# Kernel optimization log

Hardware: AMD Instinct MI355X
Metric: run time of the kernel (lower is better)

## Reference

```python
import jax, jax.numpy as jnp
import numpy as np

EMB = 300
HID = 1024
RELU = 512
NCLS = 3
T = 8192


def _lstm_layer(x, Wih, Whh, bih, bhh):
    # x: [T, in_dim]; PyTorch gate order i, f, g, o; batch = 1 so state is a vector.
    H = Whh.shape[1]
    xg = x @ Wih.T + bih  # [T, 4H], input projection hoisted out of the scan

    def step(carry, xg_t):
        h, c = carry
        gates = xg_t + Whh @ h + bhh
        i, f, g, o = jnp.split(gates, 4)
        i = jax.nn.sigmoid(i)
        f = jax.nn.sigmoid(f)
        g = jnp.tanh(g)
        o = jax.nn.sigmoid(o)
        c = f * c + i * g
        h = o * jnp.tanh(c)
        return (h, c), h

    h0 = jnp.zeros((H,), x.dtype)
    (_, _), hs = jax.lax.scan(step, (h0, h0), xg)
    return hs  # [T, H]


def setup_inputs() -> dict:
    key = jax.random.key(0)
    ks = jax.random.split(key, 16)
    s_lstm = 1.0 / np.sqrt(HID)

    def n(k, shape, s):
        return (jax.random.normal(k, shape, dtype=jnp.float32) * s)

    return {
        "quote": n(ks[0], (T, EMB), 1.0),
        "Wih0": n(ks[1], (4 * HID, EMB), s_lstm),
        "Whh0": n(ks[2], (4 * HID, HID), s_lstm),
        "bih0": n(ks[3], (4 * HID,), s_lstm),
        "bhh0": n(ks[4], (4 * HID,), s_lstm),
        "Wih1": n(ks[5], (4 * HID, HID), s_lstm),
        "Whh1": n(ks[6], (4 * HID, HID), s_lstm),
        "bih1": n(ks[7], (4 * HID,), s_lstm),
        "bhh1": n(ks[8], (4 * HID,), s_lstm),
        "W0": n(ks[9], (RELU, HID), 1.0 / np.sqrt(HID)),
        "b0": n(ks[10], (RELU,), 0.01),
        "W1": n(ks[11], (RELU, RELU), 1.0 / np.sqrt(RELU)),
        "b1": n(ks[12], (RELU,), 0.01),
        "W2": n(ks[13], (NCLS, RELU), 1.0 / np.sqrt(RELU)),
        "b2": n(ks[14], (NCLS,), 0.01),
    }


def reference(quote, Wih0, Whh0, bih0, bhh0, Wih1, Whh1, bih1, bhh1,
              W0, b0, W1, b1, W2, b2):
    h1 = _lstm_layer(quote, Wih0, Whh0, bih0, bhh0)  # [T, HID]
    h2 = _lstm_layer(h1, Wih1, Whh1, bih1, bhh1)     # [T, HID]
    last = h2[-1]                                     # lstmOut of final word, batch 1
    x = jax.nn.relu(last @ W0.T + b0)
    x = jax.nn.relu(x @ W1.T + b1)
    # Dropout(p=0.5) is identity in eval mode.
    logits = (x @ W2.T + b2).reshape(1, NCLS)
    return jax.nn.log_softmax(logits, axis=1)
```

## Files before the change

kernel.cpp:

```cpp
#include <hip/hip_runtime.h>
#include <stdint.h>

typedef unsigned int uint32;
typedef unsigned long long uint64;

#define T_SEQ 8192

#define WO_WHH0  0ull
#define WO_WIH0  8388608ull
#define WO_WHH1  10878976ull
#define WO_WIH1  19267584ull
#define WO_B0    27656192ull
#define WO_B1    27672576ull
#define WO_H1    27688960ull
#define WO_H2    27697152ull
#define WO_CST0  27705344ull
#define WO_CST1  27709440ull
#define WO_Y0    27713536ull
#define WO_Y1    27715584ull

__device__ __forceinline__ float bflo(uint32 u){ return __uint_as_float(u << 16); }
__device__ __forceinline__ float bfhi(uint32 u){ return __uint_as_float(u & 0xffff0000u); }

__device__ __forceinline__ unsigned short f2bf(float f){
  uint32 u = __float_as_uint(f);
  u += 0x7fffu + ((u >> 16) & 1u);
  return (unsigned short)(u >> 16);
}

__device__ __forceinline__ void mac8(float& a, uint4 w,
    float h0,float h1,float h2,float h3,float h4,float h5,float h6,float h7){
  a = fmaf(bflo(w.x), h0, a); a = fmaf(bfhi(w.x), h1, a);
  a = fmaf(bflo(w.y), h2, a); a = fmaf(bfhi(w.y), h3, a);
  a = fmaf(bflo(w.z), h4, a); a = fmaf(bfhi(w.z), h5, a);
  a = fmaf(bflo(w.w), h6, a); a = fmaf(bfhi(w.w), h7, a);
}

extern "C" __global__ void __launch_bounds__(256)
prep_weights(const float* __restrict__ Wih0, const float* __restrict__ Whh0,
             const float* __restrict__ bih0, const float* __restrict__ bhh0,
             const float* __restrict__ Wih1, const float* __restrict__ Whh1,
             const float* __restrict__ bih1, const float* __restrict__ bhh1,
             char* __restrict__ ws)
{
  unsigned short* whh0b = (unsigned short*)(ws + WO_WHH0);
  unsigned short* wih0b = (unsigned short*)(ws + WO_WIH0);
  unsigned short* whh1b = (unsigned short*)(ws + WO_WHH1);
  unsigned short* wih1b = (unsigned short*)(ws + WO_WIH1);
  float* b0 = (float*)(ws + WO_B0);
  float* b1 = (float*)(ws + WO_B1);

  const int stride = gridDim.x * blockDim.x;
  const int tid0 = blockIdx.x * blockDim.x + threadIdx.x;

  for (int i = tid0; i < 4096*1024; i += stride) whh0b[i] = f2bf(Whh0[i]);
  for (int i = tid0; i < 4096*1024; i += stride) whh1b[i] = f2bf(Whh1[i]);
  for (int i = tid0; i < 4096*1024; i += stride) wih1b[i] = f2bf(Wih1[i]);
  for (int i = tid0; i < 4096*304;  i += stride) {
    int r = i / 304, x = i - r * 304;
    wih0b[i] = f2bf(x < 300 ? Wih0[(size_t)r * 300 + x] : 0.0f);
  }
  for (int i = tid0; i < 4096; i += stride) {
    b0[i] = bih0[i] + bhh0[i];
    b1[i] = bih1[i] + bhh1[i];
  }
}

extern "C" __global__ void __launch_bounds__(256)
lstm_step(int t, const float* __restrict__ quote, char* __restrict__ ws)
{
  const unsigned short* whh0b = (const unsigned short*)(ws + WO_WHH0);
  const unsigned short* wih0b = (const unsigned short*)(ws + WO_WIH0);
  const unsigned short* whh1b = (const unsigned short*)(ws + WO_WHH1);
  const unsigned short* wih1b = (const unsigned short*)(ws + WO_WIH1);
  const float* b0 = (const float*)(ws + WO_B0);
  const float* b1 = (const float*)(ws + WO_B1);
  float* h1buf = (float*)(ws + WO_H1);
  float* h2buf = (float*)(ws + WO_H2);
  float* cst0  = (float*)(ws + WO_CST0);
  float* cst1  = (float*)(ws + WO_CST1);

  const int tid = threadIdx.x;
  const int wv  = tid >> 6;
  const int c   = tid & 63;

  float acc[4];
  #pragma unroll
  for (int i = 0; i < 4; ++i) acc[i] = 0.0f;

  if (blockIdx.x < 256) {
    if (t >= T_SEQ) return;
    const int u = (int)blockIdx.x * 4 + wv;

    if (c < 38) {
      float xv[8];
      int x0 = c << 3;
      const float* xr = quote + (size_t)t * 300;
      #pragma unroll
      for (int m = 0; m < 8; ++m) xv[m] = (x0 + m < 300) ? xr[x0 + m] : 0.0f;
      #pragma unroll
      for (int g = 0; g < 4; ++g) {
        int row = (g << 10) + u;
        uint4 w = *(const uint4*)(wih0b + (size_t)row * 304 + (c << 3));
        mac8(acc[g], w, xv[0],xv[1],xv[2],xv[3],xv[4],xv[5],xv[6],xv[7]);
      }
    }
    if (t > 0) {
      const float* hb = h1buf + (size_t)((t - 1) & 1) * 1024;
      float hv[16];
      #pragma unroll
      for (int k = 0; k < 16; ++k) hv[k] = hb[(c << 4) + k];
      #pragma unroll
      for (int g = 0; g < 4; ++g) {
        int row = (g << 10) + u;
        const uint4* wp = (const uint4*)(whh0b + (size_t)row * 1024 + (c << 4));
        uint4 w0 = wp[0], w1 = wp[1];
        mac8(acc[g], w0, hv[0],hv[1],hv[2],hv[3],hv[4],hv[5],hv[6],hv[7]);
        mac8(acc[g], w1, hv[8],hv[9],hv[10],hv[11],hv[12],hv[13],hv[14],hv[15]);
      }
    }
    #pragma unroll
    for (int i = 0; i < 4; ++i) {
      #pragma unroll
      for (int m = 1; m < 64; m <<= 1) acc[i] += __shfl_xor(acc[i], m);
    }
    if (c == 0) {
      float pre[4];
      #pragma unroll
      for (int g = 0; g < 4; ++g) pre[g] = acc[g] + b0[(g << 10) + u];
      float ig = 1.0f/(1.0f+expf(-pre[0])), fg = 1.0f/(1.0f+expf(-pre[1]));
      float gg = tanhf(pre[2]),             og = 1.0f/(1.0f+expf(-pre[3]));
      float cs = fg * cst0[u] + ig * gg;
      cst0[u] = cs;
      h1buf[(size_t)(t & 1) * 1024 + u] = og * tanhf(cs);
    }
  } else {
    const int s = t - 1;
    if (s < 0) return;
    const int u = ((int)blockIdx.x - 256) * 4 + wv;

    {
      const float* hb = h1buf + (size_t)(s & 1) * 1024;
      float hv[16];
      #pragma unroll
      for (int k = 0; k < 16; ++k) hv[k] = hb[(c << 4) + k];
      #pragma unroll
      for (int g = 0; g < 4; ++g) {
        int row = (g << 10) + u;
        const uint4* wp = (const uint4*)(wih1b + (size_t)row * 1024 + (c << 4));
        uint4 w0 = wp[0], w1 = wp[1];
        mac8(acc[g], w0, hv[0],hv[1],hv[2],hv[3],hv[4],hv[5],hv[6],hv[7]);
        mac8(acc[g], w1, hv[8],hv[9],hv[10],hv[11],hv[12],hv[13],hv[14],hv[15]);
      }
    }
    if (s > 0) {
      const float* hb = h2buf + (size_t)((s - 1) & 1) * 1024;
      float hv[16];
      #pragma unroll
      for (int k = 0; k < 16; ++k) hv[k] = hb[(c << 4) + k];
      #pragma unroll
      for (int g = 0; g < 4; ++g) {
        int row = (g << 10) + u;
        const uint4* wp = (const uint4*)(whh1b + (size_t)row * 1024 + (c << 4));
        uint4 w0 = wp[0], w1 = wp[1];
        mac8(acc[g], w0, hv[0],hv[1],hv[2],hv[3],hv[4],hv[5],hv[6],hv[7]);
        mac8(acc[g], w1, hv[8],hv[9],hv[10],hv[11],hv[12],hv[13],hv[14],hv[15]);
      }
    }
    #pragma unroll
    for (int i = 0; i < 4; ++i) {
      #pragma unroll
      for (int m = 1; m < 64; m <<= 1) acc[i] += __shfl_xor(acc[i], m);
    }
    if (c == 0) {
      float pre[4];
      #pragma unroll
      for (int g = 0; g < 4; ++g) pre[g] = acc[g] + b1[(g << 10) + u];
      float ig = 1.0f/(1.0f+expf(-pre[0])), fg = 1.0f/(1.0f+expf(-pre[1]));
      float gg = tanhf(pre[2]),             og = 1.0f/(1.0f+expf(-pre[3]));
      float cs = fg * cst1[u] + ig * gg;
      cst1[u] = cs;
      h2buf[(size_t)(s & 1) * 1024 + u] = og * tanhf(cs);
    }
  }
}

extern "C" __global__ void __launch_bounds__(256)
head_fc(const float* __restrict__ W, const float* __restrict__ b,
        const float* __restrict__ xin, float* __restrict__ y, int n_in)
{
  __shared__ float sred[256];
  const int i = blockIdx.x;
  float p = 0.0f;
  for (int k = threadIdx.x; k < n_in; k += 256)
    p = fmaf(W[(size_t)i * n_in + k], xin[k], p);
  sred[threadIdx.x] = p;
  __syncthreads();
  for (int s = 128; s > 0; s >>= 1) {
    if (threadIdx.x < s) sred[threadIdx.x] += sred[threadIdx.x + s];
    __syncthreads();
  }
  if (threadIdx.x == 0) y[i] = fmaxf(sred[0] + b[i], 0.0f);
}

extern "C" __global__ void __launch_bounds__(64)
head_out(const float* __restrict__ W2, const float* __restrict__ b2,
         const float* __restrict__ y1, float* __restrict__ out)
{
  const int l = threadIdx.x;
  float p0 = 0.0f, p1 = 0.0f, p2 = 0.0f;
  for (int k = l; k < 512; k += 64) {
    float v = y1[k];
    p0 = fmaf(W2[k],        v, p0);
    p1 = fmaf(W2[512 + k],  v, p1);
    p2 = fmaf(W2[1024 + k], v, p2);
  }
  #pragma unroll
  for (int m = 1; m < 64; m <<= 1) {
    p0 += __shfl_xor(p0, m);
    p1 += __shfl_xor(p1, m);
    p2 += __shfl_xor(p2, m);
  }
  if (l == 0) {
    float z0 = p0 + b2[0], z1 = p1 + b2[1], z2 = p2 + b2[2];
    float mx = fmaxf(z0, fmaxf(z1, z2));
    float lse = mx + logf(expf(z0 - mx) + expf(z1 - mx) + expf(z2 - mx));
    out[0] = z0 - lse; out[1] = z1 - lse; out[2] = z2 - lse;
  }
}

extern "C" void kernel_launch(void* const* d_in, const int* in_sizes, int n_in,
                              void* d_out, int out_size, void* d_ws, size_t ws_size,
                              hipStream_t stream)
{
  (void)in_sizes; (void)n_in; (void)out_size; (void)ws_size;
  const float* quote = (const float*)d_in[0];
  const float* Wih0  = (const float*)d_in[1];
  const float* Whh0  = (const float*)d_in[2];
  const float* bih0  = (const float*)d_in[3];
  const float* bhh0  = (const float*)d_in[4];
  const float* Wih1  = (const float*)d_in[5];
  const float* Whh1  = (const float*)d_in[6];
  const float* bih1  = (const float*)d_in[7];
  const float* bhh1  = (const float*)d_in[8];
  const float* W0    = (const float*)d_in[9];
  const float* b0    = (const float*)d_in[10];
  const float* W1    = (const float*)d_in[11];
  const float* b1    = (const float*)d_in[12];
  const float* W2    = (const float*)d_in[13];
  const float* b2    = (const float*)d_in[14];

  char* ws = (char*)d_ws;
  float* h2buf = (float*)(ws + WO_H2);
  float* y0    = (float*)(ws + WO_Y0);
  float* y1    = (float*)(ws + WO_Y1);

  hipMemsetAsync(ws + WO_CST0, 0, 8192, stream);

  prep_weights<<<2048, 256, 0, stream>>>(Wih0, Whh0, bih0, bhh0,
                                         Wih1, Whh1, bih1, bhh1, ws);

  for (int t = 0; t <= T_SEQ; ++t)
    lstm_step<<<512, 256, 0, stream>>>(t, quote, ws);

  head_fc<<<512, 256, 0, stream>>>(W0, b0, h2buf + 1024, y0, 1024);
  head_fc<<<512, 256, 0, stream>>>(W1, b1, y0, y1, 512);
  head_out<<<1, 64, 0, stream>>>(W2, b2, y1, (float*)d_out);
}
```

Baseline: 42.12 ms.

## Split layer-1 input and recurrent matvecs across waves; vectorize hidden loads

```diff
diff --git a/kernel.cpp b/kernel.cpp
--- a/kernel.cpp
+++ b/kernel.cpp
@@ -92,6 +92,15 @@
     if (t >= T_SEQ) return;
     const int u = (int)blockIdx.x * 4 + wv;
 
+    float hv[16];
+    if (t > 0) {
+      const float4* hb4 = (const float4*)(h1buf + (size_t)((t - 1) & 1) * 1024 + (c << 4));
+      float4 a0 = hb4[0], a1 = hb4[1], a2 = hb4[2], a3 = hb4[3];
+      hv[0]=a0.x; hv[1]=a0.y; hv[2]=a0.z; hv[3]=a0.w;
+      hv[4]=a1.x; hv[5]=a1.y; hv[6]=a1.z; hv[7]=a1.w;
+      hv[8]=a2.x; hv[9]=a2.y; hv[10]=a2.z; hv[11]=a2.w;
+      hv[12]=a3.x; hv[13]=a3.y; hv[14]=a3.z; hv[15]=a3.w;
+    }
     if (c < 38) {
       float xv[8];
       int x0 = c << 3;
@@ -106,10 +115,6 @@
       }
     }
     if (t > 0) {
-      const float* hb = h1buf + (size_t)((t - 1) & 1) * 1024;
-      float hv[16];
-      #pragma unroll
-      for (int k = 0; k < 16; ++k) hv[k] = hb[(c << 4) + k];
       #pragma unroll
       for (int g = 0; g < 4; ++g) {
         int row = (g << 10) + u;
@@ -135,47 +140,46 @@
       h1buf[(size_t)(t & 1) * 1024 + u] = og * tanhf(cs);
     }
   } else {
+    __shared__ float sred[16];
     const int s = t - 1;
     if (s < 0) return;
-    const int u = ((int)blockIdx.x - 256) * 4 + wv;
-
-    {
-      const float* hb = h1buf + (size_t)(s & 1) * 1024;
-      float hv[16];
-      #pragma unroll
-      for (int k = 0; k < 16; ++k) hv[k] = hb[(c << 4) + k];
+    const int lb = (int)blockIdx.x - 256;
+    const int u  = lb * 2 + (wv >> 1);
+    const int mtx = wv & 1;
+
+    const bool active = (mtx == 0) || (s > 0);
+    if (active) {
+      const float* hsrc = (mtx == 0) ? (h1buf + (size_t)(s & 1) * 1024)
+                                     : (h2buf + (size_t)((s - 1) & 1) * 1024);
+      const unsigned short* wb = (mtx == 0) ? wih1b : whh1b;
+      const float4* hb4 = (const float4*)(hsrc + (c << 4));
+      float4 a0 = hb4[0], a1 = hb4[1], a2 = hb4[2], a3 = hb4[3];
+      float hv[16] = {a0.x,a0.y,a0.z,a0.w, a1.x,a1.y,a1.z,a1.w,
+                      a2.x,a2.y,a2.z,a2.w, a3.x,a3.y,a3.z,a3.w};
       #pragma unroll
       for (int g = 0; g < 4; ++g) {
         int row = (g << 10) + u;
-        const uint4* wp = (const uint4*)(wih1b + (size_t)row * 1024 + (c << 4));
+        const uint4* wp = (const uint4*)(wb + (size_t)row * 1024 + (c << 4));
         uint4 w0 = wp[0], w1 = wp[1];
         mac8(acc[g], w0, hv[0],hv[1],hv[2],hv[3],hv[4],hv[5],hv[6],hv[7]);
         mac8(acc[g], w1, hv[8],hv[9],hv[10],hv[11],hv[12],hv[13],hv[14],hv[15]);
       }
     }
-    if (s > 0) {
-      const float* hb = h2buf + (size_t)((s - 1) & 1) * 1024;
-      float hv[16];
-      #pragma unroll
-      for (int k = 0; k < 16; ++k) hv[k] = hb[(c << 4) + k];
-      #pragma unroll
-      for (int g = 0; g < 4; ++g) {
-        int row = (g << 10) + u;
-        const uint4* wp = (const uint4*)(whh1b + (size_t)row * 1024 + (c << 4));
-        uint4 w0 = wp[0], w1 = wp[1];
-        mac8(acc[g], w0, hv[0],hv[1],hv[2],hv[3],hv[4],hv[5],hv[6],hv[7]);
-        mac8(acc[g], w1, hv[8],hv[9],hv[10],hv[11],hv[12],hv[13],hv[14],hv[15]);
-      }
-    }
     #pragma unroll
     for (int i = 0; i < 4; ++i) {
       #pragma unroll
       for (int m = 1; m < 64; m <<= 1) acc[i] += __shfl_xor(acc[i], m);
     }
     if (c == 0) {
+      #pragma unroll
+      for (int g = 0; g < 4; ++g) sred[wv * 4 + g] = acc[g];
+    }
+    __syncthreads();
+    if (mtx == 0 && c == 0) {
       float pre[4];
       #pragma unroll
-      for (int g = 0; g < 4; ++g) pre[g] = acc[g] + b1[(g << 10) + u];
+      for (int g = 0; g < 4; ++g)
+        pre[g] = acc[g] + sred[(wv + 1) * 4 + g] + b1[(g << 10) + u];
       float ig = 1.0f/(1.0f+expf(-pre[0])), fg = 1.0f/(1.0f+expf(-pre[1]));
       float gg = tanhf(pre[2]),             og = 1.0f/(1.0f+expf(-pre[3]));
       float cs = fg * cst1[u] + ig * gg;
@@ -261,7 +265,7 @@
                                          Wih1, Whh1, bih1, bhh1, ws);
 
   for (int t = 0; t <= T_SEQ; ++t)
-    lstm_step<<<512, 256, 0, stream>>>(t, quote, ws);
+    lstm_step<<<768, 256, 0, stream>>>(t, quote, ws);
 
   head_fc<<<512, 256, 0, stream>>>(W0, b0, h2buf + 1024, y0, 1024);
   head_fc<<<512, 256, 0, stream>>>(W1, b1, y0, y1, 512);
```

Result: slower. 43.11 ms (+2.3%).
